# Performance work log

Hardware: AMD Instinct MI355X
Metric: run time of the kernel (lower is better)

The kernel has to match this reference:

```python
import jax, jax.numpy as jnp
import numpy as np

D_STATE = 16


def setup_inputs() -> dict:
    key = jax.random.key(0)
    ks = jax.random.split(key, 7)
    B, S, D = 8, 4096, 64
    ds = D_STATE
    x = jax.random.normal(ks[0], (B, S, D), dtype=jnp.float32)
    # Selection layers modeled as Linear(d_model, out). W_A scaled small so the
    # random transition matrices are contractive over 4096 steps.
    W_A = jax.random.normal(ks[1], (D, ds * ds), dtype=jnp.float32) * 0.01
    b_A = jnp.zeros((ds * ds,), dtype=jnp.float32)
    W_B = jax.random.normal(ks[2], (D, ds * D), dtype=jnp.float32) * 0.05
    b_B = jnp.zeros((ds * D,), dtype=jnp.float32)
    W_C = jax.random.normal(ks[3], (D, ds * D), dtype=jnp.float32) * 0.05
    b_C = jnp.zeros((ds * D,), dtype=jnp.float32)
    return {"x": x, "W_A": W_A, "b_A": b_A, "W_B": W_B, "b_B": b_B,
            "W_C": W_C, "b_C": b_C}


def reference(x, W_A, b_A, W_B, b_B, W_C, b_C):
    B, S, D = x.shape
    ds = D_STATE
    # Input-dependent (selective) parameters per timestep
    A = (x @ W_A + b_A).reshape(B, S, ds, ds)      # [B,S,ds,ds]
    Bm = (x @ W_B + b_B).reshape(B, S, ds, D)      # [B,S,ds,D]
    Cm = (x @ W_C + b_C).reshape(B, S, ds, D)      # [B,S,ds,D]
    # Pre-contract B_t @ x_t once: [B,S,ds]
    Bx = jnp.einsum('bsnd,bsd->bsn', Bm, x)

    def step(h, inputs):
        A_t, Bx_t = inputs                          # [B,ds,ds], [B,ds]
        h = jnp.einsum('bij,bj->bi', A_t, h) + Bx_t
        return h, h

    h0 = jnp.zeros((B, ds), dtype=x.dtype)
    _, hs = jax.lax.scan(step, h0,
                         (jnp.swapaxes(A, 0, 1), jnp.swapaxes(Bx, 0, 1)))
    hs = jnp.swapaxes(hs, 0, 1)                     # [B,S,ds]
    # output_t = C_t^T @ h_t  -> [B,S,D]
    return jnp.einsum('bsnd,bsn->bsd', Cm, hs)
```

## Files before the change

kernel.cpp:

```cpp
#include <hip/hip_runtime.h>

#define BATCH   8
#define SEQ     4096
#define DM      64
#define DS      16
#define BS      (BATCH*SEQ)
#define CHUNK   16
#define NCHT    (BS/CHUNK)
#define SG      16
#define NSG     (NCHT/SG)

typedef __attribute__((ext_vector_type(8))) __bf16 bf16x8;
typedef __attribute__((ext_vector_type(4))) float  f32x4;

__device__ __forceinline__ unsigned short f2bf(float f) {
  unsigned int u = __float_as_uint(f);
  u += 0x7fffu + ((u >> 16) & 1u);
  return (unsigned short)(u >> 16);
}
__device__ __forceinline__ float bflo(unsigned int u) { return __uint_as_float(u << 16); }
__device__ __forceinline__ float bfhi(unsigned int u) { return __uint_as_float(u & 0xffff0000u); }

#define AS_I 20
#define AS_T 324

__global__ __launch_bounds__(256) void k0_castw(
    const float* __restrict__ WA, const float* __restrict__ WB,
    const float* __restrict__ WC,
    unsigned short* __restrict__ WBApk, unsigned short* __restrict__ WCpk)
{
  const int o = blockIdx.x * 256 + threadIdx.x;
  if (o < 81920) {
    int idx = o;
    const int e = idx & 7;    idx >>= 3;
    const int f = idx % 10;   idx /= 10;
    const int quad = idx & 3; idx >>= 2;
    const int l15 = idx & 15; idx >>= 4;
    const int n = idx;
    float src;
    if (f < 8) {
      const int r = f >> 1, h = f & 1;
      src = WB[(h * 32 + quad * 8 + e) * 1024 + (n * 4 + r) * 16 + l15];
    } else {
      const int h = f - 8;
      src = WA[(h * 32 + quad * 8 + e) * 256 + n * 16 + l15];
    }
    WBApk[o] = f2bf(src);
  } else {
    const int p = o - 81920;
    const int e = p & 7;
    const int h = (p >> 3) & 1;
    const int quad = (p >> 4) & 3;
    const int l15 = (p >> 6) & 15;
    const int nr = p >> 10;
    WCpk[p] = f2bf(WC[(h * 32 + quad * 8 + e) * 1024 + nr * 16 + l15]);
  }
}

struct WFrag {
  bf16x8 b00, b01, b10, b11, b20, b21, b30, b31;
  bf16x8 a0f, a1f;
  float  ba;
};

__device__ __forceinline__ WFrag loadw(
    const unsigned short* __restrict__ WBApk,
    const float* __restrict__ bA, int n, int l15, int quad)
{
  WFrag f;
  const bf16x8* fp = (const bf16x8*)(WBApk + (size_t)((n * 16 + l15) * 4 + quad) * 80);
  f.b00 = fp[0]; f.b01 = fp[1];
  f.b10 = fp[2]; f.b11 = fp[3];
  f.b20 = fp[4]; f.b21 = fp[5];
  f.b30 = fp[6]; f.b31 = fp[7];
  f.a0f = fp[8]; f.a1f = fp[9];
  f.ba  = bA[n * 16 + l15];
  return f;
}

__global__ __launch_bounds__(256, 2) void g1(
    const float* __restrict__ x, const unsigned short* __restrict__ WBApk,
    const float* __restrict__ bB,
    const float* __restrict__ bA, unsigned short* __restrict__ xb,
    unsigned short* __restrict__ Wt_ws, float* __restrict__ u_ws,
    float* __restrict__ P_ws, float* __restrict__ v_ws)
{
  __shared__ __align__(16) float xs[64][68];
  __shared__ __align__(16) float bBs[1024];
  __shared__ __align__(16) unsigned short As[64 * AS_T];
  __shared__ __align__(16) float bxs[64][16];
  __shared__ __align__(16) float us[4][16];

  const int tid  = threadIdx.x;
  const int lane = tid & 63;
  const int l15  = lane & 15;
  const int quad = lane >> 4;
  const int w    = tid >> 6;
  const int t0   = blockIdx.x * 64;
  const int twl  = w * 16;

  {
    const float4* xg = (const float4*)(x + (size_t)t0 * DM);
    #pragma unroll
    for (int i = 0; i < 4; ++i) {
      const int f4 = tid + 256 * i;
      ((float4*)&xs[f4 >> 4][0])[f4 & 15] = xg[f4];
    }
    ((float4*)bBs)[tid] = ((const float4*)bB)[tid];
    if (tid < 64) us[tid >> 4][tid & 15] = 0.f;
  }
  __syncthreads();

  WFrag cur = loadw(WBApk, bA, 0, l15, quad);

  bf16x8 a0, a1;
  {
    const int row = twl + l15;
    union { bf16x8 v; ushort4 s[2]; } ua, ub;
    float4 p0 = *(const float4*)&xs[row][quad * 8];
    float4 p1 = *(const float4*)&xs[row][quad * 8 + 4];
    float4 p2 = *(const float4*)&xs[row][32 + quad * 8];
    float4 p3 = *(const float4*)&xs[row][32 + quad * 8 + 4];
    ua.s[0] = (ushort4){f2bf(p0.x), f2bf(p0.y), f2bf(p0.z), f2bf(p0.w)};
    ua.s[1] = (ushort4){f2bf(p1.x), f2bf(p1.y), f2bf(p1.z), f2bf(p1.w)};
    ub.s[0] = (ushort4){f2bf(p2.x), f2bf(p2.y), f2bf(p2.z), f2bf(p2.w)};
    ub.s[1] = (ushort4){f2bf(p3.x), f2bf(p3.y), f2bf(p3.z), f2bf(p3.w)};
    a0 = ua.v; a1 = ub.v;
    unsigned short* xp = xb + (size_t)(t0 + row) * 64 + quad * 8;
    *(bf16x8*)xp        = a0;
    *(bf16x8*)(xp + 32) = a1;
  }

  float xv[4][4];
  #pragma unroll
  for (int r = 0; r < 4; ++r)
    #pragma unroll
    for (int reg = 0; reg < 4; ++reg)
      xv[r][reg] = xs[twl + quad * 4 + reg][r * 16 + l15];

  #pragma unroll
  for (int n = 0; n < 16; ++n) {
    WFrag nxt = (n < 15) ? loadw(WBApk, bA, n + 1, l15, quad) : cur;

    const f32x4 z4 = {0.f, 0.f, 0.f, 0.f};
    f32x4 aac = z4;
    aac = __builtin_amdgcn_mfma_f32_16x16x32_bf16(a0, cur.a0f, aac, 0, 0, 0);
    aac = __builtin_amdgcn_mfma_f32_16x16x32_bf16(a1, cur.a1f, aac, 0, 0, 0);

    f32x4 ac0 = z4, ac1 = z4, ac2 = z4, ac3 = z4;
    ac0 = __builtin_amdgcn_mfma_f32_16x16x32_bf16(a0, cur.b00, ac0, 0, 0, 0);
    ac0 = __builtin_amdgcn_mfma_f32_16x16x32_bf16(a1, cur.b01, ac0, 0, 0, 0);
    ac1 = __builtin_amdgcn_mfma_f32_16x16x32_bf16(a0, cur.b10, ac1, 0, 0, 0);
    ac1 = __builtin_amdgcn_mfma_f32_16x16x32_bf16(a1, cur.b11, ac1, 0, 0, 0);
    ac2 = __builtin_amdgcn_mfma_f32_16x16x32_bf16(a0, cur.b20, ac2, 0, 0, 0);
    ac2 = __builtin_amdgcn_mfma_f32_16x16x32_bf16(a1, cur.b21, ac2, 0, 0, 0);
    ac3 = __builtin_amdgcn_mfma_f32_16x16x32_bf16(a0, cur.b30, ac3, 0, 0, 0);
    ac3 = __builtin_amdgcn_mfma_f32_16x16x32_bf16(a1, cur.b31, ac3, 0, 0, 0);

    const float bb0 = bBs[n * 64 +  0 + l15];
    const float bb1 = bBs[n * 64 + 16 + l15];
    const float bb2 = bBs[n * 64 + 32 + l15];
    const float bb3 = bBs[n * 64 + 48 + l15];
    float part[4];
    #pragma unroll
    for (int reg = 0; reg < 4; ++reg) {
      float s = fmaf(ac0[reg] + bb0, xv[0][reg], 0.f);
      s = fmaf(ac1[reg] + bb1, xv[1][reg], s);
      s = fmaf(ac2[reg] + bb2, xv[2][reg], s);
      s = fmaf(ac3[reg] + bb3, xv[3][reg], s);
      part[reg] = s;
    }
    #pragma unroll
    for (int off = 1; off < 16; off <<= 1) {
      #pragma unroll
      for (int reg = 0; reg < 4; ++reg)
        part[reg] += __shfl_xor(part[reg], off, 64);
    }
    if (l15 == 0) {
      #pragma unroll
      for (int reg = 0; reg < 4; ++reg)
        bxs[twl + quad * 4 + reg][n] = part[reg];
    }

    As[(twl + quad * 4 + 0) * AS_T + n * AS_I + l15] = f2bf(aac[0] + cur.ba);
    As[(twl + quad * 4 + 1) * AS_T + n * AS_I + l15] = f2bf(aac[1] + cur.ba);
    As[(twl + quad * 4 + 2) * AS_T + n * AS_I + l15] = f2bf(aac[2] + cur.ba);
    As[(twl + quad * 4 + 3) * AS_T + n * AS_I + l15] = f2bf(aac[3] + cur.ba);

    cur = nxt;
  }

  {
    bf16x8 wb;
    #pragma unroll
    for (int j = 0; j < 8; ++j) wb[j] = (__bf16)((quad * 8 + j == l15) ? 1.f : 0.f);
    f32x4 d = {0.f, 0.f, 0.f, 0.f};
    const int qq = quad & 1;

    const unsigned short* rpp = &As[twl * AS_T + l15 * AS_I];
    uint2 r0 = *(const uint2*)(rpp);
    uint2 r1 = *(const uint2*)(rpp + 4);
    uint2 r2 = *(const uint2*)(rpp + 8);
    uint2 r3 = *(const uint2*)(rpp + 12);

    #pragma unroll 1
    for (int t = 0; t < CHUNK; ++t) {
      const int tl = twl + t;

      uint2 s0, s1, s2, s3;
      if (t < CHUNK - 1) {
        const unsigned short* rp = &As[(tl + 1) * AS_T + l15 * AS_I];
        s0 = *(const uint2*)(rp);
        s1 = *(const uint2*)(rp + 4);
        s2 = *(const uint2*)(rp + 8);
        s3 = *(const uint2*)(rp + 12);
      } else { s0 = r0; s1 = r1; s2 = r2; s3 = r3; }

      uint4 abits;
      if (quad == 0)      abits = make_uint4(r0.x, r0.y, r1.x, r1.y);
      else if (quad == 1) abits = make_uint4(r2.x, r2.y, r3.x, r3.y);
      else                abits = make_uint4(0u, 0u, 0u, 0u);
      bf16x8 af = *(bf16x8*)&abits;

      f32x4 z4 = {0.f, 0.f, 0.f, 0.f};
      d = __builtin_amdgcn_mfma_f32_16x16x32_bf16(af, wb, z4, 0, 0, 0);

      float nu;
      {
        float4 U0 = *(const float4*)&us[w][0];
        float4 U1 = *(const float4*)&us[w][4];
        float4 U2 = *(const float4*)&us[w][8];
        float4 U3 = *(const float4*)&us[w][12];
        float n0 = bxs[tl][l15], n1 = 0.f, n2 = 0.f, n3 = 0.f;
        n0 = fmaf(bflo(r0.x), U0.x, n0); n0 = fmaf(bfhi(r0.x), U0.y, n0);
        n0 = fmaf(bflo(r0.y), U0.z, n0); n0 = fmaf(bfhi(r0.y), U0.w, n0);
        n1 = fmaf(bflo(r1.x), U1.x, n1); n1 = fmaf(bfhi(r1.x), U1.y, n1);
        n1 = fmaf(bflo(r1.y), U1.z, n1); n1 = fmaf(bfhi(r1.y), U1.w, n1);
        n2 = fmaf(bflo(r2.x), U2.x, n2); n2 = fmaf(bfhi(r2.x), U2.y, n2);
        n2 = fmaf(bflo(r2.y), U2.z, n2); n2 = fmaf(bfhi(r2.y), U2.w, n2);
        n3 = fmaf(bflo(r3.x), U3.x, n3); n3 = fmaf(bfhi(r3.x), U3.y, n3);
        n3 = fmaf(bflo(r3.y), U3.z, n3); n3 = fmaf(bfhi(r3.y), U3.w, n3);
        nu = (n0 + n1) + (n2 + n3);
      }

      bf16x8 nb;
      nb[0] = (__bf16)__shfl(d[0], (2 * qq + 0) * 16 + l15, 64);
      nb[1] = (__bf16)__shfl(d[1], (2 * qq + 0) * 16 + l15, 64);
      nb[2] = (__bf16)__shfl(d[2], (2 * qq + 0) * 16 + l15, 64);
      nb[3] = (__bf16)__shfl(d[3], (2 * qq + 0) * 16 + l15, 64);
      nb[4] = (__bf16)__shfl(d[0], (2 * qq + 1) * 16 + l15, 64);
      nb[5] = (__bf16)__shfl(d[1], (2 * qq + 1) * 16 + l15, 64);
      nb[6] = (__bf16)__shfl(d[2], (2 * qq + 1) * 16 + l15, 64);
      nb[7] = (__bf16)__shfl(d[3], (2 * qq + 1) * 16 + l15, 64);
      wb = nb;

      if (quad == 0) {
        us[w][l15] = nu;
        bxs[tl][l15] = nu;
      }
      #pragma unroll
      for (int r = 0; r < 4; ++r)
        As[tl * AS_T + (quad * 4 + r) * AS_I + l15] = f2bf(d[r]);

      r0 = s0; r1 = s1; r2 = s2; r3 = s3;
    }

    const int chunk = blockIdx.x * 4 + w;
    #pragma unroll
    for (int r = 0; r < 4; ++r)
      P_ws[(size_t)chunk * 256 + (quad * 4 + r) * 16 + l15] = d[r];
    if (quad == 0) v_ws[(size_t)chunk * DS + l15] = us[w][l15];
  }
  __syncthreads();

  {
    uint4* Wg = (uint4*)(Wt_ws + (size_t)t0 * 256);
    #pragma unroll 1
    for (int z = 0; z < 8; ++z) {
      const int p4 = z * 256 + tid;
      const int f  = p4 * 8;
      const int t  = f >> 8, i = (f >> 4) & 15, k = f & 15;
      const unsigned short* sp = &As[t * AS_T + i * AS_I + k];
      uint2 lo = *(const uint2*)(sp);
      uint2 hi = *(const uint2*)(sp + 4);
      Wg[p4] = make_uint4(lo.x, lo.y, hi.x, hi.y);
    }
    ((float4*)(u_ws + (size_t)t0 * DS))[tid] = ((const float4*)&bxs[0][0])[tid];
  }
}

__global__ __launch_bounds__(1024, 4) void k3f(
    const float* __restrict__ P_ws, const float* __restrict__ v_ws,
    float* __restrict__ hb_ws,
    const unsigned short* __restrict__ Wt_ws,
    const unsigned short* __restrict__ xb,
    const float* __restrict__ u_ws)
{
  __shared__ float Qs[16][256];
  __shared__ float wsv[16][16];
  __shared__ float hbgs[16][16];

  const int tid = threadIdx.x;
  const int bx  = blockIdx.x;

  if (bx >= 8) {
    const uint4* wp = (const uint4*)(Wt_ws + (size_t)bx * 32 * 256);
    uint4 a = wp[tid];
    const unsigned int* xp = (const unsigned int*)(xb + (size_t)bx * 32 * 64);
    unsigned int b = xp[tid];
    unsigned int c = 0;
    if (tid < 512) c = ((const unsigned int*)(u_ws + (size_t)bx * 32 * DS))[tid];
    asm volatile("" :: "v"(a.x), "v"(b), "v"(c));
    return;
  }

  const int lane = tid & 63;
  const int l15  = lane & 15;
  const int quad = lane >> 4;
  const int wv   = tid >> 6;
  const int qq   = quad & 1;

  {
    const int s = bx * 16 + wv;
    if (lane < 16) wsv[wv][lane] = 0.f;
    bf16x8 wb;
    #pragma unroll
    for (int j = 0; j < 8; ++j) wb[j] = (__bf16)((quad * 8 + j == l15) ? 1.f : 0.f);
    f32x4 d = {0.f, 0.f, 0.f, 0.f};

    float4 p0 = {0.f,0.f,0.f,0.f}, p1 = {0.f,0.f,0.f,0.f};
    float nv;
    {
      const int chunk = s * SG;
      if (quad < 2) {
        const float4* pr = (const float4*)(P_ws + (size_t)chunk * 256 + l15 * 16 + quad * 8);
        p0 = pr[0]; p1 = pr[1];
      }
      nv = v_ws[(size_t)chunk * DS + l15];
    }

    #pragma unroll 1
    for (int t = 0; t < SG; ++t) {
      float4 q0 = {0.f,0.f,0.f,0.f}, q1 = {0.f,0.f,0.f,0.f};
      float nv2 = 0.f;
      if (t < SG - 1) {
        const int chunk = s * SG + t + 1;
        if (quad < 2) {
          const float4* pr = (const float4*)(P_ws + (size_t)chunk * 256 + l15 * 16 + quad * 8);
          q0 = pr[0]; q1 = pr[1];
        }
        nv2 = v_ws[(size_t)chunk * DS + l15];
      }

      bf16x8 af;
      af[0] = (__bf16)p0.x; af[1] = (__bf16)p0.y; af[2] = (__bf16)p0.z; af[3] = (__bf16)p0.w;
      af[4] = (__bf16)p1.x; af[5] = (__bf16)p1.y; af[6] = (__bf16)p1.z; af[7] = (__bf16)p1.w;

      f32x4 z4 = {0.f, 0.f, 0.f, 0.f};
      d = __builtin_amdgcn_mfma_f32_16x16x32_bf16(af, wb, z4, 0, 0, 0);

      float part = 0.f;
      if (quad < 2) {
        const float* wrow = &wsv[wv][quad * 8];
        part = p0.x*wrow[0] + p0.y*wrow[1] + p0.z*wrow[2] + p0.w*wrow[3]
             + p1.x*wrow[4] + p1.y*wrow[5] + p1.z*wrow[6] + p1.w*wrow[7];
      }
      part += __shfl_xor(part, 16, 64);

      bf16x8 nb;
      nb[0] = (__bf16)__shfl(d[0], (2 * qq + 0) * 16 + l15, 64);
      nb[1] = (__bf16)__shfl(d[1], (2 * qq + 0) * 16 + l15, 64);
      nb[2] = (__bf16)__shfl(d[2], (2 * qq + 0) * 16 + l15, 64);
      nb[3] = (__bf16)__shfl(d[3], (2 * qq + 0) * 16 + l15, 64);
      nb[4] = (__bf16)__shfl(d[0], (2 * qq + 1) * 16 + l15, 64);
      nb[5] = (__bf16)__shfl(d[1], (2 * qq + 1) * 16 + l15, 64);
      nb[6] = (__bf16)__shfl(d[2], (2 * qq + 1) * 16 + l15, 64);
      nb[7] = (__bf16)__shfl(d[3], (2 * qq + 1) * 16 + l15, 64);
      wb = nb;

      if (quad == 0) wsv[wv][l15] = part + nv;

      p0 = q0; p1 = q1; nv = nv2;
    }

    #pragma unroll
    for (int r = 0; r < 4; ++r)
      Qs[wv][(quad * 4 + r) * 16 + l15] = d[r];
  }
  __syncthreads();

  if (tid < 16) {
    const int r = tid;
    float h = 0.f;
    #pragma unroll 1
    for (int g = 0; g < 16; ++g) {
      hbgs[g][r] = h;
      const float4* Pr = (const float4*)&Qs[g][r * 16];
      float4 c0 = Pr[0], c1 = Pr[1], c2 = Pr[2], c3 = Pr[3];
      const float vc = wsv[g][r];
      float a0 = c0.x*__shfl(h, 0,16) + c0.y*__shfl(h, 1,16) + c0.z*__shfl(h, 2,16) + c0.w*__shfl(h, 3,16);
      float a1 = c1.x*__shfl(h, 4,16) + c1.y*__shfl(h, 5,16) + c1.z*__shfl(h, 6,16) + c1.w*__shfl(h, 7,16);
      float a2 = c2.x*__shfl(h, 8,16) + c2.y*__shfl(h, 9,16) + c2.z*__shfl(h,10,16) + c2.w*__shfl(h,11,16);
      float a3 = c3.x*__shfl(h,12,16) + c3.y*__shfl(h,13,16) + c3.z*__shfl(h,14,16) + c3.w*__shfl(h,15,16);
      h = vc + ((a0 + a1) + (a2 + a3));
    }
  }
  __syncthreads();

  if (tid < 256) {
    const int g = tid >> 4;
    const int r = tid & 15;
    const int s = bx * 16 + g;
    float h = hbgs[g][r];

    float4 c0, c1, c2, c3; float vc;
    {
      const int chunk = s * SG;
      const float4* Pr = (const float4*)&P_ws[(size_t)chunk * 256 + r * 16];
      c0 = Pr[0]; c1 = Pr[1]; c2 = Pr[2]; c3 = Pr[3];
      vc = v_ws[(size_t)chunk * DS + r];
    }

    #pragma unroll 1
    for (int t = 0; t < SG; ++t) {
      const int chunk = s * SG + t;
      float4 d0, d1, d2, d3; float vc2;
      if (t < SG - 1) {
        const float4* Pr = (const float4*)&P_ws[(size_t)(chunk + 1) * 256 + r * 16];
        d0 = Pr[0]; d1 = Pr[1]; d2 = Pr[2]; d3 = Pr[3];
        vc2 = v_ws[(size_t)(chunk + 1) * DS + r];
      } else { d0 = c0; d1 = c1; d2 = c2; d3 = c3; vc2 = vc; }

      hb_ws[(size_t)chunk * DS + r] = h;
      float a0 = c0.x*__shfl(h, 0,16) + c0.y*__shfl(h, 1,16) + c0.z*__shfl(h, 2,16) + c0.w*__shfl(h, 3,16);
      float a1 = c1.x*__shfl(h, 4,16) + c1.y*__shfl(h, 5,16) + c1.z*__shfl(h, 6,16) + c1.w*__shfl(h, 7,16);
      float a2 = c2.x*__shfl(h, 8,16) + c2.y*__shfl(h, 9,16) + c2.z*__shfl(h,10,16) + c2.w*__shfl(h,11,16);
      float a3 = c3.x*__shfl(h,12,16) + c3.y*__shfl(h,13,16) + c3.z*__shfl(h,14,16) + c3.w*__shfl(h,15,16);
      h = vc + ((a0 + a1) + (a2 + a3));

      c0 = d0; c1 = d1; c2 = d2; c3 = d3; vc = vc2;
    }
  }
}

__global__ __launch_bounds__(256, 6) void g2(
    const unsigned short* __restrict__ xb, const unsigned short* __restrict__ WCpk,
    const float* __restrict__ bC, const unsigned short* __restrict__ Wt_ws,
    const float* __restrict__ u_ws, const float* __restrict__ hb_ws,
    float* __restrict__ out)
{
  __shared__ float hsh[16][17];
  __shared__ float bCs[1024];
  const int tid  = threadIdx.x;
  const int lane = tid & 63;
  const int l15  = lane & 15;
  const int quad = lane >> 4;
  const int w    = tid >> 6;
  const int t0   = blockIdx.x * 16;
  const int rc   = w;

  ((float4*)bCs)[tid] = ((const float4*)bC)[tid];

  const bf16x8* xvp = (const bf16x8*)(xb + (size_t)(t0 + l15) * 64);
  bf16x8 a0 = xvp[quad];
  bf16x8 a1 = xvp[quad + 4];

  const int tl = tid >> 4, i = tid & 15;
  const int t  = t0 + tl;
  const uint4* wr = (const uint4*)(Wt_ws + (size_t)t * 256 + i * 16);
  uint4 wa = wr[0], wbv = wr[1];
  const float4* hp = (const float4*)(hb_ws + (size_t)blockIdx.x * DS);
  float4 h0 = hp[0], h1 = hp[1], h2 = hp[2], h3 = hp[3];
  float uu = u_ws[(size_t)t * DS + i];
  {
    float p0 = uu, p1 = 0.f, p2 = 0.f, p3 = 0.f;
    p0 = fmaf(bflo(wa.x),  h0.x, p0); p0 = fmaf(bfhi(wa.x),  h0.y, p0);
    p0 = fmaf(bflo(wa.y),  h0.z, p0); p0 = fmaf(bfhi(wa.y),  h0.w, p0);
    p1 = fmaf(bflo(wa.z),  h1.x, p1); p1 = fmaf(bfhi(wa.z),  h1.y, p1);
    p1 = fmaf(bflo(wa.w),  h1.z, p1); p1 = fmaf(bfhi(wa.w),  h1.w, p1);
    p2 = fmaf(bflo(wbv.x), h2.x, p2); p2 = fmaf(bfhi(wbv.x), h2.y, p2);
    p2 = fmaf(bflo(wbv.y), h2.z, p2); p2 = fmaf(bfhi(wbv.y), h2.w, p2);
    p3 = fmaf(bflo(wbv.z), h3.x, p3); p3 = fmaf(bfhi(wbv.z), h3.y, p3);
    p3 = fmaf(bflo(wbv.w), h3.z, p3); p3 = fmaf(bfhi(wbv.w), h3.w, p3);
    hsh[tl][i] = (p0 + p1) + (p2 + p3);
  }
  __syncthreads();

  f32x4 o0 = {0.f, 0.f, 0.f, 0.f};

  const bf16x8* cp = (const bf16x8*)(WCpk + (size_t)((0 * 4 + rc) * 64 + l15 * 4 + quad) * 16);
  bf16x8 c00 = cp[0], c01 = cp[1];
  #pragma unroll
  for (int n = 0; n < 16; ++n) {
    bf16x8 n00 = c00, n01 = c01;
    if (n < 15) {
      const bf16x8* np = (const bf16x8*)(WCpk + (size_t)(((n + 1) * 4 + rc) * 64 + l15 * 4 + quad) * 16);
      n00 = np[0]; n01 = np[1];
    }

    f32x4 ac0 = {0.f, 0.f, 0.f, 0.f};
    ac0 = __builtin_amdgcn_mfma_f32_16x16x32_bf16(a0, c00, ac0, 0, 0, 0);
    ac0 = __builtin_amdgcn_mfma_f32_16x16x32_bf16(a1, c01, ac0, 0, 0, 0);

    float hn[4];
    #pragma unroll
    for (int reg = 0; reg < 4; ++reg) hn[reg] = hsh[quad * 4 + reg][n];

    const float bc0 = bCs[n * 64 + rc * 16 + l15];
    #pragma unroll
    for (int reg = 0; reg < 4; ++reg)
      o0[reg] = fmaf(ac0[reg] + bc0, hn[reg], o0[reg]);

    c00 = n00; c01 = n01;
  }

  #pragma unroll
  for (int reg = 0; reg < 4; ++reg)
    out[(size_t)(t0 + quad * 4 + reg) * DM + rc * 16 + l15] = o0[reg];
}

extern "C" void kernel_launch(void* const* d_in, const int* in_sizes, int n_in,
                              void* d_out, int out_size, void* d_ws, size_t ws_size,
                              hipStream_t stream) {
  const float* x  = (const float*)d_in[0];
  const float* WA = (const float*)d_in[1];
  const float* bA = (const float*)d_in[2];
  const float* WB = (const float*)d_in[3];
  const float* bB = (const float*)d_in[4];
  const float* WC = (const float*)d_in[5];
  const float* bC = (const float*)d_in[6];
  float* out = (float*)d_out;

  float* ws     = (float*)d_ws;
  float* P_ws   = ws;
  float* v_ws   = P_ws   + (size_t)NCHT * 256;
  float* u_ws   = v_ws   + (size_t)NCHT * DS;
  float* Q_ws   = u_ws   + (size_t)BS * DS;
  float* w_ws   = Q_ws   + (size_t)NSG * 256;
  float* hbg_ws = w_ws   + (size_t)NSG * DS;
  float* hb_ws  = hbg_ws + (size_t)NSG * DS;
  unsigned short* xb    = (unsigned short*)(hb_ws + (size_t)NCHT * DS);
  unsigned short* WBApk = xb    + (size_t)BS * 64;
  unsigned short* WCpk  = WBApk + 81920;
  unsigned short* Wt_ws = WCpk  + 65536;

  k0_castw<<<576,      256, 0, stream>>>(WA, WB, WC, WBApk, WCpk);
  g1      <<<BS / 64,  256, 0, stream>>>(x, WBApk, bB, bA, xb, Wt_ws, u_ws, P_ws, v_ws);
  k3f     <<<1024,    1024, 0, stream>>>(P_ws, v_ws, hb_ws, Wt_ws, xb, u_ws);
  g2      <<<BS / 16,  256, 0, stream>>>(xb, WCpk, bC, Wt_ws, u_ws, hb_ws, out);
}
```

Baseline: 175.0 us.

## Recompute per-step transition matrices in g2 instead of storing them to workspace

New measurement: 197.2 us. 12.7% more time.

```diff
diff --git a/kernel.cpp b/kernel.cpp
--- a/kernel.cpp
+++ b/kernel.cpp
@@ -82,7 +82,7 @@
     const float* __restrict__ x, const unsigned short* __restrict__ WBApk,
     const float* __restrict__ bB,
     const float* __restrict__ bA, unsigned short* __restrict__ xb,
-    unsigned short* __restrict__ Wt_ws, float* __restrict__ u_ws,
+    float* __restrict__ u_ws,
     float* __restrict__ P_ws, float* __restrict__ v_ws)
 {
   __shared__ __align__(16) float xs[64][68];
@@ -254,13 +254,7 @@
       nb[7] = (__bf16)__shfl(d[3], (2 * qq + 1) * 16 + l15, 64);
       wb = nb;
 
-      if (quad == 0) {
-        us[w][l15] = nu;
-        bxs[tl][l15] = nu;
-      }
-      #pragma unroll
-      for (int r = 0; r < 4; ++r)
-        As[tl * AS_T + (quad * 4 + r) * AS_I + l15] = f2bf(d[r]);
+      if (quad == 0) us[w][l15] = nu;
 
       r0 = s0; r1 = s1; r2 = s2; r3 = s3;
     }
@@ -273,26 +267,12 @@
   }
   __syncthreads();
 
-  {
-    uint4* Wg = (uint4*)(Wt_ws + (size_t)t0 * 256);
-    #pragma unroll 1
-    for (int z = 0; z < 8; ++z) {
-      const int p4 = z * 256 + tid;
-      const int f  = p4 * 8;
-      const int t  = f >> 8, i = (f >> 4) & 15, k = f & 15;
-      const unsigned short* sp = &As[t * AS_T + i * AS_I + k];
-      uint2 lo = *(const uint2*)(sp);
-      uint2 hi = *(const uint2*)(sp + 4);
-      Wg[p4] = make_uint4(lo.x, lo.y, hi.x, hi.y);
-    }
-    ((float4*)(u_ws + (size_t)t0 * DS))[tid] = ((const float4*)&bxs[0][0])[tid];
-  }
+  ((float4*)(u_ws + (size_t)t0 * DS))[tid] = ((const float4*)&bxs[0][0])[tid];
 }
 
 __global__ __launch_bounds__(1024, 4) void k3f(
     const float* __restrict__ P_ws, const float* __restrict__ v_ws,
     float* __restrict__ hb_ws,
-    const unsigned short* __restrict__ Wt_ws,
     const unsigned short* __restrict__ xb,
     const float* __restrict__ u_ws)
 {
@@ -304,13 +284,11 @@
   const int bx  = blockIdx.x;
 
   if (bx >= 8) {
-    const uint4* wp = (const uint4*)(Wt_ws + (size_t)bx * 32 * 256);
-    uint4 a = wp[tid];
     const unsigned int* xp = (const unsigned int*)(xb + (size_t)bx * 32 * 64);
     unsigned int b = xp[tid];
     unsigned int c = 0;
     if (tid < 512) c = ((const unsigned int*)(u_ws + (size_t)bx * 32 * DS))[tid];
-    asm volatile("" :: "v"(a.x), "v"(b), "v"(c));
+    asm volatile("" :: "v"(b), "v"(c));
     return;
   }
 
@@ -445,10 +423,12 @@
 
 __global__ __launch_bounds__(256, 6) void g2(
     const unsigned short* __restrict__ xb, const unsigned short* __restrict__ WCpk,
-    const float* __restrict__ bC, const unsigned short* __restrict__ Wt_ws,
-    const float* __restrict__ u_ws, const float* __restrict__ hb_ws,
-    float* __restrict__ out)
+    const float* __restrict__ bC, const unsigned short* __restrict__ WBApk,
+    const float* __restrict__ bA, const float* __restrict__ u_ws,
+    const float* __restrict__ hb_ws, float* __restrict__ out)
 {
+  __shared__ __align__(16) unsigned short As[16 * AS_T];
+  __shared__ float bxls[16][16];
   __shared__ float hsh[16][17];
   __shared__ float bCs[1024];
   const int tid  = threadIdx.x;
@@ -460,29 +440,51 @@
   const int rc   = w;
 
   ((float4*)bCs)[tid] = ((const float4*)bC)[tid];
+  bxls[tid >> 4][tid & 15] = u_ws[(size_t)(t0 + (tid >> 4)) * DS + (tid & 15)];
 
   const bf16x8* xvp = (const bf16x8*)(xb + (size_t)(t0 + l15) * 64);
   bf16x8 a0 = xvp[quad];
   bf16x8 a1 = xvp[quad + 4];
 
-  const int tl = tid >> 4, i = tid & 15;
-  const int t  = t0 + tl;
-  const uint4* wr = (const uint4*)(Wt_ws + (size_t)t * 256 + i * 16);
-  uint4 wa = wr[0], wbv = wr[1];
-  const float4* hp = (const float4*)(hb_ws + (size_t)blockIdx.x * DS);
-  float4 h0 = hp[0], h1 = hp[1], h2 = hp[2], h3 = hp[3];
-  float uu = u_ws[(size_t)t * DS + i];
-  {
-    float p0 = uu, p1 = 0.f, p2 = 0.f, p3 = 0.f;
-    p0 = fmaf(bflo(wa.x),  h0.x, p0); p0 = fmaf(bfhi(wa.x),  h0.y, p0);
-    p0 = fmaf(bflo(wa.y),  h0.z, p0); p0 = fmaf(bfhi(wa.y),  h0.w, p0);
-    p1 = fmaf(bflo(wa.z),  h1.x, p1); p1 = fmaf(bfhi(wa.z),  h1.y, p1);
-    p1 = fmaf(bflo(wa.w),  h1.z, p1); p1 = fmaf(bfhi(wa.w),  h1.w, p1);
-    p2 = fmaf(bflo(wbv.x), h2.x, p2); p2 = fmaf(bfhi(wbv.x), h2.y, p2);
-    p2 = fmaf(bflo(wbv.y), h2.z, p2); p2 = fmaf(bfhi(wbv.y), h2.w, p2);
-    p3 = fmaf(bflo(wbv.z), h3.x, p3); p3 = fmaf(bfhi(wbv.z), h3.y, p3);
-    p3 = fmaf(bflo(wbv.w), h3.z, p3); p3 = fmaf(bfhi(wbv.w), h3.w, p3);
-    hsh[tl][i] = (p0 + p1) + (p2 + p3);
+  #pragma unroll
+  for (int j = 0; j < 4; ++j) {
+    const int n = w * 4 + j;
+    const unsigned short* fp = WBApk + (size_t)((n * 16 + l15) * 4 + quad) * 80;
+    bf16x8 wa0 = *(const bf16x8*)(fp + 64);
+    bf16x8 wa1 = *(const bf16x8*)(fp + 72);
+    f32x4 aac = {0.f, 0.f, 0.f, 0.f};
+    aac = __builtin_amdgcn_mfma_f32_16x16x32_bf16(a0, wa0, aac, 0, 0, 0);
+    aac = __builtin_amdgcn_mfma_f32_16x16x32_bf16(a1, wa1, aac, 0, 0, 0);
+    const float ba = bA[n * 16 + l15];
+    As[(quad * 4 + 0) * AS_T + n * AS_I + l15] = f2bf(aac[0] + ba);
+    As[(quad * 4 + 1) * AS_T + n * AS_I + l15] = f2bf(aac[1] + ba);
+    As[(quad * 4 + 2) * AS_T + n * AS_I + l15] = f2bf(aac[2] + ba);
+    As[(quad * 4 + 3) * AS_T + n * AS_I + l15] = f2bf(aac[3] + ba);
+  }
+  __syncthreads();
+
+  if (w == 0) {
+    const float* hbp = hb_ws + (size_t)blockIdx.x * DS;
+    float hk0 = hbp[quad * 4 + 0];
+    float hk1 = hbp[quad * 4 + 1];
+    float hk2 = hbp[quad * 4 + 2];
+    float hk3 = hbp[quad * 4 + 3];
+    #pragma unroll 1
+    for (int t = 0; t < CHUNK; ++t) {
+      uint2 ar = *(const uint2*)&As[t * AS_T + l15 * AS_I + quad * 4];
+      float p = fmaf(bflo(ar.x), hk0, 0.f);
+      p = fmaf(bfhi(ar.x), hk1, p);
+      p = fmaf(bflo(ar.y), hk2, p);
+      p = fmaf(bfhi(ar.y), hk3, p);
+      p += __shfl_xor(p, 16, 64);
+      p += __shfl_xor(p, 32, 64);
+      const float hnew = p + bxls[t][l15];
+      if (quad == 0) hsh[t][l15] = hnew;
+      hk0 = __shfl(hnew, quad * 4 + 0, 64);
+      hk1 = __shfl(hnew, quad * 4 + 1, 64);
+      hk2 = __shfl(hnew, quad * 4 + 2, 64);
+      hk3 = __shfl(hnew, quad * 4 + 3, 64);
+    }
   }
   __syncthreads();
 
@@ -542,10 +544,9 @@
   unsigned short* xb    = (unsigned short*)(hb_ws + (size_t)NCHT * DS);
   unsigned short* WBApk = xb    + (size_t)BS * 64;
   unsigned short* WCpk  = WBApk + 81920;
-  unsigned short* Wt_ws = WCpk  + 65536;
 
   k0_castw<<<576,      256, 0, stream>>>(WA, WB, WC, WBApk, WCpk);
-  g1      <<<BS / 64,  256, 0, stream>>>(x, WBApk, bB, bA, xb, Wt_ws, u_ws, P_ws, v_ws);
-  k3f     <<<1024,    1024, 0, stream>>>(P_ws, v_ws, hb_ws, Wt_ws, xb, u_ws);
-  g2      <<<BS / 16,  256, 0, stream>>>(xb, WCpk, bC, Wt_ws, u_ws, hb_ws, out);
-}
+  g1      <<<BS / 64,  256, 0, stream>>>(x, WBApk, bB, bA, xb, u_ws, P_ws, v_ws);
+  k3f     <<<1024,    1024, 0, stream>>>(P_ws, v_ws, hb_ws, xb, u_ws);
+  g2      <<<BS / 16,  256, 0, stream>>>(xb, WCpk, bC, WBApk, bA, u_ws, hb_ws, out);
+}
```
